# Optimization experiments

Hardware: AMD Instinct MI355X
Metric: run time of the kernel (lower is better)

## Reference

```python
import jax, jax.numpy as jnp
import numpy as np

B, T, D, U = 32, 2048, 1024, 1024


def setup_inputs() -> dict:
    key = jax.random.key(0)
    ks = jax.random.split(key, 6)
    scale = 0.02
    return {
        "query": jax.random.normal(ks[0], (B, D), jnp.float32),
        "values": jax.random.normal(ks[1], (B, T, D), jnp.float32),
        "W1_k": jax.random.normal(ks[2], (D, U), jnp.float32) * scale,
        "W1_b": jnp.zeros((U,), jnp.float32),
        "W2_k": jax.random.normal(ks[3], (D, U), jnp.float32) * scale,
        "W2_b": jnp.zeros((U,), jnp.float32),
        "V_k": jax.random.normal(ks[4], (U, 1), jnp.float32) * scale,
        "V_b": jnp.zeros((1,), jnp.float32),
    }


def reference(query, values, W1_k, W1_b, W2_k, W2_b, V_k, V_b):
    # query: [B, D] -> [B, 1, U]; values: [B, T, D] -> [B, T, U]
    q_proj = (query @ W1_k + W1_b)[:, None, :]
    v_proj = jnp.einsum("btd,du->btu", values, W2_k) + W2_b
    # score: [B, T, 1]
    score = jnp.tanh(q_proj + v_proj) @ V_k + V_b
    attention_weights = jax.nn.softmax(score, axis=1)  # over time axis T
    context_vector = jnp.sum(attention_weights * values, axis=1)  # [B, D]
    return context_vector
```

## Files before the change

kernel.cpp:

```cpp
#include <hip/hip_runtime.h>

#define NB 32
#define NT 2048
#define ND 1024
#define NU 1024
#define NM (NB*NT)

using f32x4 = __attribute__((ext_vector_type(4))) float;
using s16x8 = __attribute__((ext_vector_type(8))) short;

#define BAR()   asm volatile("s_barrier" ::: "memory")
#define LGKM0() asm volatile("s_waitcnt lgkmcnt(0)" ::: "memory")
#define VMC(n)  asm volatile("s_waitcnt vmcnt(" #n ")" ::: "memory")
#define SB0()   __builtin_amdgcn_sched_barrier(0)

__device__ __forceinline__ unsigned short f2bf(float f) {
  unsigned u = __builtin_bit_cast(unsigned, f);
  u = u + 0x7fffu + ((u >> 16) & 1u);
  return (unsigned short)(u >> 16);
}

__device__ __forceinline__ void gload_lds16(const void* g, void* l) {
  __builtin_amdgcn_global_load_lds(
      (const __attribute__((address_space(1))) unsigned int*)g,
      (__attribute__((address_space(3))) unsigned int*)l, 16, 0, 0);
}

__device__ __forceinline__ float tanh_fast(float x) {
  float e = __expf(2.0f * x);
  return 1.0f - 2.0f * __builtin_amdgcn_rcpf(e + 1.0f);
}

__device__ __forceinline__ void stage_tile(const unsigned short* g, unsigned short* l,
                                           int w, int lane) {
  int l2 = lane >> 2;
  int gc = (lane & 3) ^ ((lane >> 3) & 3);
#pragma unroll
  for (int i = 0; i < 2; ++i) {
    int rblk = w * 2 + i;
    int row = rblk * 16 + l2;
    gload_lds16(g + (size_t)row * 1024 + gc * 8, l + rblk * 512);
  }
}

__device__ __forceinline__ s16x8 frag_read(const unsigned short* buf, int row, int lg) {
  int cr = lg ^ ((row >> 1) & 3);
  return *(const s16x8*)(buf + row * 32 + cr * 8);
}

#define MFMA16(MB, FA) \
  _Pragma("unroll") \
  for (int m = 0; m < 4; ++m) { \
    _Pragma("unroll") \
    for (int n = 0; n < 4; ++n) \
      acc[(MB) + m][n] = __builtin_amdgcn_mfma_f32_16x16x32_bf16( \
          FA[m], fb[n], acc[(MB) + m][n], 0, 0, 0); \
  }

template<bool PRE, bool ST, int VM>
__device__ __forceinline__ void tile_body(
    int kt, const unsigned short* gA, const unsigned short* gB,
    unsigned short* sA, unsigned short* sB, f32x4 (&acc)[8][4],
    s16x8 (&fa03)[4], s16x8 (&fa47)[4], s16x8 (&fb)[4],
    int w, int lane, int wr, int wc, int l15, int lg) {
  const unsigned short* pA = sA + (kt & 3) * 8192;
  const unsigned short* qA = sA + ((kt + 1) & 3) * 8192;
  const unsigned short* qB = sB + ((kt + 1) & 3) * 8192;
  unsigned short* stA = sA + ((kt + 3) & 3) * 8192;
  unsigned short* stB = sB + ((kt + 3) & 3) * 8192;
  LGKM0(); SB0();
  __builtin_amdgcn_s_setprio(1);
  MFMA16(0, fa03);
  __builtin_amdgcn_s_setprio(0);
  SB0();
#pragma unroll
  for (int i = 0; i < 4; ++i)
    fa47[i] = frag_read(pA, wr * 128 + (4 + i) * 16 + l15, lg);
  if (ST) stage_tile(gA + (size_t)(kt + 3) * 32, stA, w, lane);
  if constexpr (VM == 6) { VMC(6); }
  else if constexpr (VM == 4) { VMC(4); }
  else if constexpr (VM == 0) { VMC(0); }
  BAR();
  LGKM0(); SB0();
  __builtin_amdgcn_s_setprio(1);
  MFMA16(4, fa47);
  __builtin_amdgcn_s_setprio(0);
  SB0();
  if (PRE) {
#pragma unroll
    for (int i = 0; i < 4; ++i)
      fa03[i] = frag_read(qA, wr * 128 + i * 16 + l15, lg);
#pragma unroll
    for (int n = 0; n < 4; ++n)
      fb[n] = frag_read(qB, wc * 64 + n * 16 + l15, lg);
  }
  if (ST) stage_tile(gB + (size_t)(kt + 3) * 32, stB, w, lane);
  BAR();
}

__global__ __launch_bounds__(512, 2) void k_score_gemm32(
    const unsigned short* __restrict__ vbf, const unsigned short* __restrict__ W2t,
    const float* __restrict__ add2, const float* __restrict__ Vk,
    float* __restrict__ score_part) {
  __shared__ unsigned short sA[32768];
  __shared__ unsigned short sB[32768];
  const int tid = threadIdx.x;
  const int w = tid >> 6, lane = tid & 63;
  const int wr = w >> 2, wc = w & 3;
  const int l15 = lane & 15, lg = lane >> 4;

  const int L = blockIdx.x;
  const int g = (L & 7) * 128 + (L >> 3);
  const int mtile = g >> 2, ntile = g & 3;

  const unsigned short* gA = vbf + ((size_t)mtile << 18);
  const unsigned short* gB = W2t + ((size_t)ntile << 18);

  f32x4 acc[8][4] = {};
  s16x8 fa03[4], fa47[4], fb[4];

  stage_tile(gA, sA, w, lane);              stage_tile(gB, sB, w, lane);
  stage_tile(gA + 32, sA + 8192, w, lane);  stage_tile(gB + 32, sB + 8192, w, lane);
  stage_tile(gA + 64, sA + 16384, w, lane); stage_tile(gB + 64, sB + 16384, w, lane);
  VMC(8);
  BAR();
#pragma unroll
  for (int i = 0; i < 4; ++i) fa03[i] = frag_read(sA, wr * 128 + i * 16 + l15, lg);
#pragma unroll
  for (int n = 0; n < 4; ++n) fb[n] = frag_read(sB, wc * 64 + n * 16 + l15, lg);

#pragma unroll 1
  for (int kt = 0; kt < 29; ++kt)
    tile_body<true, true, 6>(kt, gA, gB, sA, sB, acc, fa03, fa47, fb, w, lane, wr, wc, l15, lg);
  tile_body<true, false, 4>(29, gA, gB, sA, sB, acc, fa03, fa47, fb, w, lane, wr, wc, l15, lg);
  tile_body<true, false, 0>(30, gA, gB, sA, sB, acc, fa03, fa47, fb, w, lane, wr, wc, l15, lg);
  tile_body<false, false, -1>(31, gA, gB, sA, sB, acc, fa03, fa47, fb, w, lane, wr, wc, l15, lg);

  const int b = (mtile * 256) >> 11;
  float vks[4], adds[4];
#pragma unroll
  for (int n = 0; n < 4; ++n) {
    int u = ntile * 256 + wc * 64 + n * 16 + l15;
    vks[n] = Vk[u];
    adds[n] = add2[(b << 10) + u];
  }
  __syncthreads();
  float* part = (float*)sA;
#pragma unroll
  for (int m = 0; m < 8; ++m) {
#pragma unroll
    for (int j = 0; j < 4; ++j) {
      float s = 0.f;
#pragma unroll
      for (int n = 0; n < 4; ++n) {
        float x = acc[m][n][j] + adds[n];
        s = fmaf(tanh_fast(x), vks[n], s);
      }
#pragma unroll
      for (int off = 1; off < 16; off <<= 1) s += __shfl_xor(s, off);
      if (l15 == 0) part[wc * 256 + wr * 128 + m * 16 + lg * 4 + j] = s;
    }
  }
  __syncthreads();
  if (tid < 256) {
    float v = part[tid] + part[256 + tid] + part[512 + tid] + part[768 + tid];
    score_part[((size_t)ntile << 16) + mtile * 256 + tid] = v;
  }
}

__global__ void k_qproj(const float* __restrict__ q, const float* __restrict__ W1,
                        const float* __restrict__ W1b, const float* __restrict__ W2b,
                        float* __restrict__ add2) {
  int u = blockIdx.x * 256 + threadIdx.x;
  int b = blockIdx.y;
  const float* qr = q + (b << 10);
  float s = 0.f;
#pragma unroll 8
  for (int d = 0; d < ND; ++d) s = fmaf(qr[d], W1[d * NU + u], s);
  add2[(b << 10) + u] = s + W1b[u] + W2b[u];
}

__global__ void k_w2t(const float* __restrict__ W2, unsigned short* __restrict__ W2t) {
  __shared__ unsigned short tile[64][65];
  int bu = blockIdx.x * 64, bd = blockIdx.y * 64;
  int x = threadIdx.x & 63, y4 = threadIdx.x >> 6;
#pragma unroll
  for (int r = 0; r < 16; ++r) {
    int dl = y4 * 16 + r;
    tile[x][dl] = f2bf(W2[(size_t)(bd + dl) * NU + bu + x]);
  }
  __syncthreads();
#pragma unroll
  for (int r = 0; r < 16; ++r) {
    int ul = y4 * 16 + r;
    W2t[(size_t)(bu + ul) * ND + bd + x] = tile[ul][x];
  }
}

__global__ void k_cvt_values(const float4* __restrict__ v, ushort4* __restrict__ o) {
  const int n4 = NM * ND / 4;
  for (int i = blockIdx.x * blockDim.x + threadIdx.x; i < n4; i += gridDim.x * blockDim.x) {
    float4 f = v[i];
    ushort4 h;
    h.x = f2bf(f.x); h.y = f2bf(f.y); h.z = f2bf(f.z); h.w = f2bf(f.w);
    o[i] = h;
  }
}

__global__ __launch_bounds__(256) void k_score_gemm_small(
    const float* __restrict__ values, const unsigned short* __restrict__ W2t,
    const float* __restrict__ add2, const float* __restrict__ Vk,
    float* __restrict__ score_part) {
  __shared__ unsigned short sA[128 * 64];
  __shared__ unsigned short sB[128 * 64];
  const int tid = threadIdx.x;
  const int w = tid >> 6, lane = tid & 63;
  const int wr = w >> 1, wc = w & 1;
  const int l15 = lane & 15, lg = lane >> 4;
  const int r8 = lane >> 3, c8 = lane & 7;
  const int cs8 = c8 ^ r8;
  const int L = blockIdx.x;
  const int mtile = (L & 7) * 64 + ((L >> 3) >> 3);
  const int ntile = (L >> 3) & 7;
  f32x4 acc[4][4] = {};
  for (int kk = 0; kk < 16; ++kk) {
    const int k0 = kk * 64;
#pragma unroll
    for (int i = 0; i < 4; ++i) {
      int nl = (w * 4 + i) * 8 + r8;
      gload_lds16(W2t + ((size_t)(ntile * 128 + nl) << 10) + k0 + cs8 * 8, sB + (w * 4 + i) * 512);
    }
#pragma unroll
    for (int i = 0; i < 8; ++i) {
      int idx = tid + (i << 8);
      int row = idx >> 4, kc = idx & 15;
      const float4 f = *(const float4*)(values + ((size_t)(mtile * 128 + row) << 10) + k0 + kc * 4);
      ushort4 h;
      h.x = f2bf(f.x); h.y = f2bf(f.y); h.z = f2bf(f.z); h.w = f2bf(f.w);
      int cc = (kc >> 1) ^ (row & 7);
      *(ushort4*)(sA + (row << 6) + cc * 8 + (kc & 1) * 4) = h;
    }
    __syncthreads();
#pragma unroll
    for (int ks = 0; ks < 2; ++ks) {
      s16x8 af[4], bfr[4];
#pragma unroll
      for (int m = 0; m < 4; ++m) {
        int row = wr * 64 + m * 16 + l15;
        int cc = (ks * 4 + lg) ^ (l15 & 7);
        af[m] = *(const s16x8*)(sA + (row << 6) + cc * 8);
      }
#pragma unroll
      for (int n = 0; n < 4; ++n) {
        int row = wc * 64 + n * 16 + l15;
        int cc = (ks * 4 + lg) ^ (l15 & 7);
        bfr[n] = *(const s16x8*)(sB + (row << 6) + cc * 8);
      }
#pragma unroll
      for (int m = 0; m < 4; ++m)
#pragma unroll
        for (int n = 0; n < 4; ++n)
          acc[m][n] = __builtin_amdgcn_mfma_f32_16x16x32_bf16(af[m], bfr[n], acc[m][n], 0, 0, 0);
    }
    __syncthreads();
  }
  const int b = (mtile * 128) >> 11;
  float vks[4], adds[4];
#pragma unroll
  for (int n = 0; n < 4; ++n) {
    int u = ntile * 128 + wc * 64 + n * 16 + l15;
    vks[n] = Vk[u];
    adds[n] = add2[(b << 10) + u];
  }
  float rs[4][4];
#pragma unroll
  for (int m = 0; m < 4; ++m)
#pragma unroll
    for (int j = 0; j < 4; ++j) {
      float s = 0.f;
#pragma unroll
      for (int n = 0; n < 4; ++n) {
        float x = acc[m][n][j] + adds[n];
        s = fmaf(tanh_fast(x), vks[n], s);
      }
#pragma unroll
      for (int off = 1; off < 16; off <<= 1) s += __shfl_xor(s, off);
      rs[m][j] = s;
    }
  __syncthreads();
  float* rowsum = (float*)sA;
  if (wc == 0 && l15 == 0)
#pragma unroll
    for (int m = 0; m < 4; ++m)
#pragma unroll
      for (int j = 0; j < 4; ++j) rowsum[wr * 64 + m * 16 + lg * 4 + j] = rs[m][j];
  __syncthreads();
  if (wc == 1 && l15 == 0)
#pragma unroll
    for (int m = 0; m < 4; ++m)
#pragma unroll
      for (int j = 0; j < 4; ++j) rowsum[wr * 64 + m * 16 + lg * 4 + j] += rs[m][j];
  __syncthreads();
  if (tid < 128)
    score_part[((size_t)ntile << 16) + mtile * 128 + tid] = rowsum[tid];
}

__global__ void k_softmax(const float* __restrict__ sp, float* __restrict__ w, int npart) {
  __shared__ float redm[4], reds[4];
  int b = blockIdx.x, tid = threadIdx.x;
  float s[8];
  float mx = -1e30f;
#pragma unroll
  for (int i = 0; i < 8; ++i) {
    int t = i * 256 + tid;
    float v = 0.f;
    for (int p = 0; p < npart; ++p) v += sp[((size_t)p << 16) + (b << 11) + t];
    s[i] = v;
    mx = fmaxf(mx, v);
  }
#pragma unroll
  for (int o = 1; o < 64; o <<= 1) mx = fmaxf(mx, __shfl_xor(mx, o));
  if ((tid & 63) == 0) redm[tid >> 6] = mx;
  __syncthreads();
  mx = fmaxf(fmaxf(redm[0], redm[1]), fmaxf(redm[2], redm[3]));
  float sum = 0.f;
#pragma unroll
  for (int i = 0; i < 8; ++i) { s[i] = __expf(s[i] - mx); sum += s[i]; }
#pragma unroll
  for (int o = 1; o < 64; o <<= 1) sum += __shfl_xor(sum, o);
  if ((tid & 63) == 0) reds[tid >> 6] = sum;
  __syncthreads();
  float inv = 1.0f / (reds[0] + reds[1] + reds[2] + reds[3]);
#pragma unroll
  for (int i = 0; i < 8; ++i) w[(b << 11) + i * 256 + tid] = s[i] * inv;
}

__global__ void k_context(const float* __restrict__ values, const float* __restrict__ wv,
                          float* __restrict__ part) {
  int d4 = threadIdx.x;
  int b = blockIdx.y, tc = blockIdx.z;
  const float4* vb = (const float4*)(values + ((size_t)b << 21) + ((size_t)tc << 18)) + d4;
  const float* wb = wv + (b << 11) + (tc << 8);
  float ax = 0.f, ay = 0.f, az = 0.f, aw = 0.f;
#pragma unroll 4
  for (int t = 0; t < 256; ++t) {
    float4 v = vb[(size_t)t << 8];
    float wt = wb[t];
    ax = fmaf(wt, v.x, ax); ay = fmaf(wt, v.y, ay);
    az = fmaf(wt, v.z, az); aw = fmaf(wt, v.w, aw);
  }
  float4* po = (float4*)(part + (((size_t)tc * NB + b) << 10)) + d4;
  *po = make_float4(ax, ay, az, aw);
}

__global__ void k_ctx_reduce(const float* __restrict__ part, float* __restrict__ out) {
  int i = blockIdx.x * 256 + threadIdx.x;
  float s = 0.f;
#pragma unroll
  for (int p = 0; p < 8; ++p) s += part[(p << 15) + i];
  out[i] = s;
}

extern "C" void kernel_launch(void* const* d_in, const int* in_sizes, int n_in,
                              void* d_out, int out_size, void* d_ws, size_t ws_size,
                              hipStream_t stream) {
  const float* query  = (const float*)d_in[0];
  const float* values = (const float*)d_in[1];
  const float* W1k    = (const float*)d_in[2];
  const float* W1b    = (const float*)d_in[3];
  const float* W2k    = (const float*)d_in[4];
  const float* W2b    = (const float*)d_in[5];
  const float* Vk     = (const float*)d_in[6];
  float* out = (float*)d_out;
  char* ws = (char*)d_ws;

  size_t off = 0;
  float* add2 = (float*)(ws + off); off += (size_t)NB * NU * 4;
  float* sp   = (float*)(ws + off); off += (size_t)8 * NM * 4;
  float* wv   = (float*)(ws + off); off += (size_t)NM * 4;
  float* ctxp = (float*)(ws + off); off += (size_t)8 * NB * ND * 4;
  unsigned short* W2t = (unsigned short*)(ws + off); off += (size_t)NU * ND * 2;
  unsigned short* vbf = (unsigned short*)(ws + off);
  size_t need_big = off + (size_t)NM * ND * 2;
  bool big = ws_size >= need_big;

  k_qproj<<<dim3(4, 32), 256, 0, stream>>>(query, W1k, W1b, W2b, add2);
  k_w2t<<<dim3(16, 16), 256, 0, stream>>>(W2k, W2t);
  if (big) {
    k_cvt_values<<<dim3(2048), 256, 0, stream>>>((const float4*)values, (ushort4*)vbf);
    k_score_gemm32<<<dim3(1024), 512, 0, stream>>>(vbf, W2t, add2, Vk, sp);
    k_softmax<<<dim3(32), 256, 0, stream>>>(sp, wv, 4);
  } else {
    k_score_gemm_small<<<dim3(4096), 256, 0, stream>>>(values, W2t, add2, Vk, sp);
    k_softmax<<<dim3(32), 256, 0, stream>>>(sp, wv, 8);
  }
  k_context<<<dim3(1, 32, 8), 256, 0, stream>>>(values, wv, ctxp);
  k_ctx_reduce<<<dim3(128), 256, 0, stream>>>(ctxp, out);
}
```

Measured before the change: 351.6 us.

## Restructure GEMM main loop to one barrier per k-tile with register double-buffering

The bf16 score GEMM inner loop is reorganised so each k-tile issues all 32 MFMAs in a single block, with one barrier per tile instead of two. The next tile's A and B fragments are read from LDS into a second register set before the current tile's MFMAs, replacing the split half-tile scheme and its explicit lgkmcnt waits. Both global-to-LDS stages for tile kt+3 are now issued together, and the vmcnt thresholds are adjusted to match. This aims to cut synchronisation overhead and hide LDS latency behind MFMA work. It roughly doubles the fragment registers held per thread, which risks spills or lower occupancy under the 512-thread, 2-block launch bound.

```diff
diff --git a/kernel.cpp b/kernel.cpp
--- a/kernel.cpp
+++ b/kernel.cpp
@@ -10,7 +10,6 @@
 using s16x8 = __attribute__((ext_vector_type(8))) short;
 
 #define BAR()   asm volatile("s_barrier" ::: "memory")
-#define LGKM0() asm volatile("s_waitcnt lgkmcnt(0)" ::: "memory")
 #define VMC(n)  asm volatile("s_waitcnt vmcnt(" #n ")" ::: "memory")
 #define SB0()   __builtin_amdgcn_sched_barrier(0)
 
@@ -48,57 +47,40 @@
   return *(const s16x8*)(buf + row * 32 + cr * 8);
 }
 
-#define MFMA16(MB, FA) \
-  _Pragma("unroll") \
-  for (int m = 0; m < 4; ++m) { \
-    _Pragma("unroll") \
-    for (int n = 0; n < 4; ++n) \
-      acc[(MB) + m][n] = __builtin_amdgcn_mfma_f32_16x16x32_bf16( \
-          FA[m], fb[n], acc[(MB) + m][n], 0, 0, 0); \
-  }
-
 template<bool PRE, bool ST, int VM>
-__device__ __forceinline__ void tile_body(
+__device__ __forceinline__ void tile_one(
     int kt, const unsigned short* gA, const unsigned short* gB,
     unsigned short* sA, unsigned short* sB, f32x4 (&acc)[8][4],
-    s16x8 (&fa03)[4], s16x8 (&fa47)[4], s16x8 (&fb)[4],
+    s16x8 (&fa)[8], s16x8 (&fb)[4], s16x8 (&nfa)[8], s16x8 (&nfb)[4],
     int w, int lane, int wr, int wc, int l15, int lg) {
-  const unsigned short* pA = sA + (kt & 3) * 8192;
-  const unsigned short* qA = sA + ((kt + 1) & 3) * 8192;
-  const unsigned short* qB = sB + ((kt + 1) & 3) * 8192;
-  unsigned short* stA = sA + ((kt + 3) & 3) * 8192;
-  unsigned short* stB = sB + ((kt + 3) & 3) * 8192;
-  LGKM0(); SB0();
+  if (PRE) {
+    const unsigned short* qA = sA + ((kt + 1) & 3) * 8192;
+    const unsigned short* qB = sB + ((kt + 1) & 3) * 8192;
+#pragma unroll
+    for (int i = 0; i < 8; ++i) nfa[i] = frag_read(qA, wr * 128 + i * 16 + l15, lg);
+#pragma unroll
+    for (int n = 0; n < 4; ++n) nfb[n] = frag_read(qB, wc * 64 + n * 16 + l15, lg);
+  }
+  SB0();
   __builtin_amdgcn_s_setprio(1);
-  MFMA16(0, fa03);
+#pragma unroll
+  for (int m = 0; m < 8; ++m)
+#pragma unroll
+    for (int n = 0; n < 4; ++n)
+      acc[m][n] = __builtin_amdgcn_mfma_f32_16x16x32_bf16(fa[m], fb[n], acc[m][n], 0, 0, 0);
   __builtin_amdgcn_s_setprio(0);
-  SB0();
-#pragma unroll
-  for (int i = 0; i < 4; ++i)
-    fa47[i] = frag_read(pA, wr * 128 + (4 + i) * 16 + l15, lg);
-  if (ST) stage_tile(gA + (size_t)(kt + 3) * 32, stA, w, lane);
-  if constexpr (VM == 6) { VMC(6); }
-  else if constexpr (VM == 4) { VMC(4); }
+  if (ST) {
+    unsigned short* stA = sA + ((kt + 3) & 3) * 8192;
+    unsigned short* stB = sB + ((kt + 3) & 3) * 8192;
+    stage_tile(gA + (size_t)(kt + 3) * 32, stA, w, lane);
+    stage_tile(gB + (size_t)(kt + 3) * 32, stB, w, lane);
+  }
+  if constexpr (VM == 4) { VMC(4); }
   else if constexpr (VM == 0) { VMC(0); }
   BAR();
-  LGKM0(); SB0();
-  __builtin_amdgcn_s_setprio(1);
-  MFMA16(4, fa47);
-  __builtin_amdgcn_s_setprio(0);
-  SB0();
-  if (PRE) {
-#pragma unroll
-    for (int i = 0; i < 4; ++i)
-      fa03[i] = frag_read(qA, wr * 128 + i * 16 + l15, lg);
-#pragma unroll
-    for (int n = 0; n < 4; ++n)
-      fb[n] = frag_read(qB, wc * 64 + n * 16 + l15, lg);
-  }
-  if (ST) stage_tile(gB + (size_t)(kt + 3) * 32, stB, w, lane);
-  BAR();
-}
-
-__global__ __launch_bounds__(512, 2) void k_score_gemm32(
+}
+
+__global__ __launch_bounds__(512, 2) void k_score_gemm1(
     const unsigned short* __restrict__ vbf, const unsigned short* __restrict__ W2t,
     const float* __restrict__ add2, const float* __restrict__ Vk,
     float* __restrict__ score_part) {
@@ -117,24 +99,27 @@
   const unsigned short* gB = W2t + ((size_t)ntile << 18);
 
   f32x4 acc[8][4] = {};
-  s16x8 fa03[4], fa47[4], fb[4];
+  s16x8 fa0[8], fb0[4], fa1[8], fb1[4];
 
   stage_tile(gA, sA, w, lane);              stage_tile(gB, sB, w, lane);
   stage_tile(gA + 32, sA + 8192, w, lane);  stage_tile(gB + 32, sB + 8192, w, lane);
   stage_tile(gA + 64, sA + 16384, w, lane); stage_tile(gB + 64, sB + 16384, w, lane);
-  VMC(8);
+  VMC(4);
   BAR();
 #pragma unroll
-  for (int i = 0; i < 4; ++i) fa03[i] = frag_read(sA, wr * 128 + i * 16 + l15, lg);
-#pragma unroll
-  for (int n = 0; n < 4; ++n) fb[n] = frag_read(sB, wc * 64 + n * 16 + l15, lg);
+  for (int i = 0; i < 8; ++i) fa0[i] = frag_read(sA, wr * 128 + i * 16 + l15, lg);
+#pragma unroll
+  for (int n = 0; n < 4; ++n) fb0[n] = frag_read(sB, wc * 64 + n * 16 + l15, lg);
 
 #pragma unroll 1
-  for (int kt = 0; kt < 29; ++kt)
-    tile_body<true, true, 6>(kt, gA, gB, sA, sB, acc, fa03, fa47, fb, w, lane, wr, wc, l15, lg);
-  tile_body<true, false, 4>(29, gA, gB, sA, sB, acc, fa03, fa47, fb, w, lane, wr, wc, l15, lg);
-  tile_body<true, false, 0>(30, gA, gB, sA, sB, acc, fa03, fa47, fb, w, lane, wr, wc, l15, lg);
-  tile_body<false, false, -1>(31, gA, gB, sA, sB, acc, fa03, fa47, fb, w, lane, wr, wc, l15, lg);
+  for (int kt = 0; kt < 28; kt += 2) {
+    tile_one<true, true, 4>(kt,     gA, gB, sA, sB, acc, fa0, fb0, fa1, fb1, w, lane, wr, wc, l15, lg);
+    tile_one<true, true, 4>(kt + 1, gA, gB, sA, sB, acc, fa1, fb1, fa0, fb0, w, lane, wr, wc, l15, lg);
+  }
+  tile_one<true,  true,  4>(28, gA, gB, sA, sB, acc, fa0, fb0, fa1, fb1, w, lane, wr, wc, l15, lg);
+  tile_one<true,  false, 0>(29, gA, gB, sA, sB, acc, fa1, fb1, fa0, fb0, w, lane, wr, wc, l15, lg);
+  tile_one<true,  false,-1>(30, gA, gB, sA, sB, acc, fa0, fb0, fa1, fb1, w, lane, wr, wc, l15, lg);
+  tile_one<false, false,-1>(31, gA, gB, sA, sB, acc, fa1, fb1, fa0, fb0, w, lane, wr, wc, l15, lg);
 
   const int b = (mtile * 256) >> 11;
   float vks[4], adds[4];
@@ -388,7 +373,7 @@
   k_w2t<<<dim3(16, 16), 256, 0, stream>>>(W2k, W2t);
   if (big) {
     k_cvt_values<<<dim3(2048), 256, 0, stream>>>((const float4*)values, (ushort4*)vbf);
-    k_score_gemm32<<<dim3(1024), 512, 0, stream>>>(vbf, W2t, add2, Vk, sp);
+    k_score_gemm1<<<dim3(1024), 512, 0, stream>>>(vbf, W2t, add2, Vk, sp);
     k_softmax<<<dim3(32), 256, 0, stream>>>(sp, wv, 4);
   } else {
     k_score_gemm_small<<<dim3(4096), 256, 0, stream>>>(values, W2t, add2, Vk, sp);
```

Measured after the change: 365.9 us. 1.04x slower.
